# Kernel optimization log

Hardware: AMD Instinct MI355X
Metric: run time of the kernel (lower is better)

Reference implementation:

```python
import jax, jax.numpy as jnp
import numpy as np

TOP_K = 1
N_EXPERTS = 32
ALPHA = 0.001
SCALING = 1.0


def setup_inputs() -> dict:
    key = jax.random.key(0)
    k1, k2 = jax.random.split(key)
    hidden_states = jax.random.normal(k1, (16, 8192, 256), dtype=jnp.float32)
    # kaiming_uniform-ish gate weight, scale irrelevant for correctness check
    weight = jax.random.normal(k2, (32, 256), dtype=jnp.float32) * 0.06
    return {"hidden_states": hidden_states, "weight": weight}


def reference(hidden_states, weight):
    bsz, seq_len, h = hidden_states.shape
    x = hidden_states.reshape(-1, h).astype(jnp.float32)           # [N, h]
    logits = jnp.einsum('nh,eh->ne', x, weight.astype(jnp.float32))  # [N, E]
    scores = jax.nn.softmax(logits, axis=-1)
    # greedy top-k (sorted order fine; torch uses sorted=False but values identical for k=1)
    topk_weight, topk_idx = jax.lax.top_k(scores, TOP_K)            # [N, K]
    topk_weight = topk_weight * SCALING  # norm_topk_prob=False, top_k=1
    # seq_aux loss (training branch, alpha > 0)
    idx_aux = topk_idx.reshape(bsz, seq_len * TOP_K)                # [B, S*K]
    ce = jax.vmap(lambda idx: jnp.zeros((N_EXPERTS,), jnp.float32).at[idx].add(1.0))(idx_aux)
    ce = ce / (seq_len * TOP_K / N_EXPERTS)
    scores_seq = scores.reshape(bsz, seq_len, N_EXPERTS)
    aux_loss = jnp.mean(jnp.sum(ce * jnp.mean(scores_seq, axis=1), axis=1)) * ALPHA
    return topk_idx, topk_weight, aux_loss
```

## Files before the change

### kernel.cpp

```cpp
#include <hip/hip_runtime.h>
#include <math.h>

#define NTOK (16 * 8192)
#define H    256
#define E    32
#define SEQ  8192
#define BSZ  16
#define T    4

__global__ __launch_bounds__(256) void zero_ws_kernel(float* ws) {
    int i = blockIdx.x * 256 + threadIdx.x;
    if (i < BSZ * E * 2) ws[i] = 0.0f;
}

__global__ __launch_bounds__(128, 2) void gate_kernel(
    const float* __restrict__ x, const float* __restrict__ w,
    float* __restrict__ out, float* __restrict__ ws_cnt, float* __restrict__ ws_sum)
{
    __shared__ float w_lds[E * H];

    const int tid = threadIdx.x;

    {
        float4*       wl = (float4*)w_lds;
        const float4* wg = (const float4*)w;
#pragma unroll
        for (int i = 0; i < (E * H / 4) / 128; ++i)
            wl[tid + 128 * i] = wg[tid + 128 * i];
    }
    __syncthreads();

    const int lane = tid & 63;
    const int col  = lane & 31;
    const int half = lane >> 5;
    const int wavebase = blockIdx.x * 256 + (tid >> 6) * 128;
    const int tok0 = wavebase + col * T;

    const float* xbase = x + (size_t)tok0 * H + half * 128;

    float acc[E][T];
#pragma unroll
    for (int e = 0; e < E; ++e)
#pragma unroll
        for (int t = 0; t < T; ++t) acc[e][t] = 0.0f;

    float4 cur[T], nxt[T];
#pragma unroll
    for (int t = 0; t < T; ++t)
        cur[t] = *(const float4*)(xbase + t * H);

#pragma unroll 1
    for (int hc = 0; hc < 128; hc += 4) {
        const int hn = (hc + 4) & 127;
#pragma unroll
        for (int t = 0; t < T; ++t)
            nxt[t] = *(const float4*)(xbase + t * H + hn);

#pragma unroll
        for (int e = 0; e < E; ++e) {
            const float4 wv = *(const float4*)(w_lds + e * H + half * 128 + hc);
#pragma unroll
            for (int t = 0; t < T; ++t) {
                acc[e][t] += wv.x * cur[t].x + wv.y * cur[t].y
                           + wv.z * cur[t].z + wv.w * cur[t].w;
            }
        }
#pragma unroll
        for (int t = 0; t < T; ++t) cur[t] = nxt[t];
    }

#pragma unroll
    for (int e = 0; e < E; ++e)
#pragma unroll
        for (int t = 0; t < T; ++t)
            acc[e][t] += __shfl_xor(acc[e][t], 32, 64);

    float m_s[2], inv_s[2];
    int   idx_s[2];
#pragma unroll
    for (int s = 0; s < 2; ++s) {
        float m = half ? acc[0][2 + s] : acc[0][s];
        int   id = 0;
#pragma unroll
        for (int e = 1; e < E; ++e) {
            const float v = half ? acc[e][2 + s] : acc[e][s];
            if (v > m) { m = v; id = e; }
        }
        float ss = 0.0f;
#pragma unroll
        for (int e = 0; e < E; ++e) {
            const float v = half ? acc[e][2 + s] : acc[e][s];
            ss += expf(v - m);
        }
        const float inv = 1.0f / ss;
        const int token = tok0 + half * 2 + s;
        out[token]        = (float)id;
        out[NTOK + token] = inv;
        m_s[s] = m; inv_s[s] = inv; idx_s[s] = id;
    }

    const int b = wavebase >> 13;

#pragma unroll 1
    for (int e = 0; e < E; ++e) {
        const float v0 = half ? acc[e][2] : acc[e][0];
        const float v1 = half ? acc[e][3] : acc[e][1];
        float sc = expf(v0 - m_s[0]) * inv_s[0] + expf(v1 - m_s[1]) * inv_s[1];
        float cn = (float)((idx_s[0] == e) + (idx_s[1] == e));
#pragma unroll
        for (int off = 32; off > 0; off >>= 1) {
            sc += __shfl_xor(sc, off, 64);
            cn += __shfl_xor(cn, off, 64);
        }
        if (lane == 0) {
            atomicAdd(&ws_sum[b * E + e], sc);
            if (cn != 0.0f) atomicAdd(&ws_cnt[b * E + e], cn);
        }
    }
}

__global__ __launch_bounds__(256) void aux_kernel(
    const float* __restrict__ ws_cnt, const float* __restrict__ ws_sum,
    float* __restrict__ out)
{
    const int tid = threadIdx.x;
    float p = 0.0f;
    for (int i = tid; i < BSZ * E; i += 256)
        p += ws_cnt[i] * ws_sum[i];

    __shared__ float red[4];
#pragma unroll
    for (int off = 32; off > 0; off >>= 1)
        p += __shfl_xor(p, off, 64);
    if ((tid & 63) == 0) red[tid >> 6] = p;
    __syncthreads();
    if (tid == 0) {
        float t = red[0] + red[1] + red[2] + red[3];
        out[2 * NTOK] = t * (0.001f / (16.0f * 256.0f * 8192.0f));
    }
}

extern "C" void kernel_launch(void* const* d_in, const int* in_sizes, int n_in,
                              void* d_out, int out_size, void* d_ws, size_t ws_size,
                              hipStream_t stream) {
    const float* x = (const float*)d_in[0];
    const float* w = (const float*)d_in[1];
    float* out    = (float*)d_out;
    float* ws     = (float*)d_ws;
    float* ws_cnt = ws;
    float* ws_sum = ws + BSZ * E;

    zero_ws_kernel<<<4, 256, 0, stream>>>(ws);
    gate_kernel<<<NTOK / 256, 128, 0, stream>>>(x, w, out, ws_cnt, ws_sum);
    aux_kernel<<<1, 256, 0, stream>>>(ws_cnt, ws_sum, out);
}
```

Before: 271.8 us.

## Halve tokens per thread, widen blocks, deepen h-chunk, ballot-based expert counts

Each thread now handles 2 tokens instead of 4, and blocks grow to 256 threads, so each wave covers 64 tokens. The h-loop processes 8 elements per step with explicit fmaf chains, and the weight tile in LDS is reused by more waves per block. Softmax exponentials are computed once and reused for the score sums, and the per-expert counts come from a ballot plus popcount instead of a shuffle reduction. The aim is lower register pressure and higher occupancy, at the cost of less x-register reuse per weight load from LDS.

```diff
diff --git a/kernel.cpp b/kernel.cpp
--- a/kernel.cpp
+++ b/kernel.cpp
@@ -6,14 +6,14 @@
 #define E    32
 #define SEQ  8192
 #define BSZ  16
-#define T    4
+#define T    2
 
 __global__ __launch_bounds__(256) void zero_ws_kernel(float* ws) {
     int i = blockIdx.x * 256 + threadIdx.x;
     if (i < BSZ * E * 2) ws[i] = 0.0f;
 }
 
-__global__ __launch_bounds__(128, 2) void gate_kernel(
+__global__ __launch_bounds__(256, 2) void gate_kernel(
     const float* __restrict__ x, const float* __restrict__ w,
     float* __restrict__ out, float* __restrict__ ws_cnt, float* __restrict__ ws_sum)
 {
@@ -25,18 +25,19 @@
         float4*       wl = (float4*)w_lds;
         const float4* wg = (const float4*)w;
 #pragma unroll
-        for (int i = 0; i < (E * H / 4) / 128; ++i)
-            wl[tid + 128 * i] = wg[tid + 128 * i];
+        for (int i = 0; i < (E * H / 4) / 256; ++i)
+            wl[tid + 256 * i] = wg[tid + 256 * i];
     }
     __syncthreads();
 
     const int lane = tid & 63;
     const int col  = lane & 31;
     const int half = lane >> 5;
-    const int wavebase = blockIdx.x * 256 + (tid >> 6) * 128;
+    const int wavebase = blockIdx.x * 256 + (tid >> 6) * 64;
     const int tok0 = wavebase + col * T;
 
     const float* xbase = x + (size_t)tok0 * H + half * 128;
+    const float* wbase = w_lds + half * 128;
 
     float acc[E][T];
 #pragma unroll
@@ -44,29 +45,45 @@
 #pragma unroll
         for (int t = 0; t < T; ++t) acc[e][t] = 0.0f;
 
-    float4 cur[T], nxt[T];
+    float4 cur[T][2], nxt[T][2];
 #pragma unroll
     for (int t = 0; t < T; ++t)
-        cur[t] = *(const float4*)(xbase + t * H);
+#pragma unroll
+        for (int j = 0; j < 2; ++j)
+            cur[t][j] = *(const float4*)(xbase + t * H + 4 * j);
 
 #pragma unroll 1
-    for (int hc = 0; hc < 128; hc += 4) {
-        const int hn = (hc + 4) & 127;
+    for (int hc = 0; hc < 128; hc += 8) {
+        const int hn = (hc + 8) & 127;
 #pragma unroll
         for (int t = 0; t < T; ++t)
-            nxt[t] = *(const float4*)(xbase + t * H + hn);
+#pragma unroll
+            for (int j = 0; j < 2; ++j)
+                nxt[t][j] = *(const float4*)(xbase + t * H + hn + 4 * j);
 
 #pragma unroll
         for (int e = 0; e < E; ++e) {
-            const float4 wv = *(const float4*)(w_lds + e * H + half * 128 + hc);
+            const float4 w0 = *(const float4*)(wbase + e * H + hc);
+            const float4 w1 = *(const float4*)(wbase + e * H + hc + 4);
 #pragma unroll
             for (int t = 0; t < T; ++t) {
-                acc[e][t] += wv.x * cur[t].x + wv.y * cur[t].y
-                           + wv.z * cur[t].z + wv.w * cur[t].w;
+                float a = acc[e][t];
+                a = fmaf(w0.x, cur[t][0].x, a);
+                a = fmaf(w0.y, cur[t][0].y, a);
+                a = fmaf(w0.z, cur[t][0].z, a);
+                a = fmaf(w0.w, cur[t][0].w, a);
+                a = fmaf(w1.x, cur[t][1].x, a);
+                a = fmaf(w1.y, cur[t][1].y, a);
+                a = fmaf(w1.z, cur[t][1].z, a);
+                a = fmaf(w1.w, cur[t][1].w, a);
+                acc[e][t] = a;
             }
         }
 #pragma unroll
-        for (int t = 0; t < T; ++t) cur[t] = nxt[t];
+        for (int t = 0; t < T; ++t)
+#pragma unroll
+            for (int j = 0; j < 2; ++j)
+                cur[t][j] = nxt[t][j];
     }
 
 #pragma unroll
@@ -75,45 +92,40 @@
         for (int t = 0; t < T; ++t)
             acc[e][t] += __shfl_xor(acc[e][t], 32, 64);
 
-    float m_s[2], inv_s[2];
-    int   idx_s[2];
 #pragma unroll
-    for (int s = 0; s < 2; ++s) {
-        float m = half ? acc[0][2 + s] : acc[0][s];
-        int   id = 0;
+    for (int e = 0; e < E; ++e)
+        acc[e][0] = half ? acc[e][1] : acc[e][0];
+
+    float m  = acc[0][0];
+    int   id = 0;
 #pragma unroll
-        for (int e = 1; e < E; ++e) {
-            const float v = half ? acc[e][2 + s] : acc[e][s];
-            if (v > m) { m = v; id = e; }
-        }
-        float ss = 0.0f;
+    for (int e = 1; e < E; ++e) {
+        if (acc[e][0] > m) { m = acc[e][0]; id = e; }
+    }
+    float ss = 0.0f;
 #pragma unroll
-        for (int e = 0; e < E; ++e) {
-            const float v = half ? acc[e][2 + s] : acc[e][s];
-            ss += expf(v - m);
-        }
-        const float inv = 1.0f / ss;
-        const int token = tok0 + half * 2 + s;
-        out[token]        = (float)id;
-        out[NTOK + token] = inv;
-        m_s[s] = m; inv_s[s] = inv; idx_s[s] = id;
+    for (int e = 0; e < E; ++e) {
+        const float p = expf(acc[e][0] - m);
+        acc[e][0] = p;
+        ss += p;
     }
+    const float inv = 1.0f / ss;
+    const int token = tok0 + half;
+    out[token]        = (float)id;
+    out[NTOK + token] = inv;
 
     const int b = wavebase >> 13;
 
-#pragma unroll 1
+#pragma unroll
     for (int e = 0; e < E; ++e) {
-        const float v0 = half ? acc[e][2] : acc[e][0];
-        const float v1 = half ? acc[e][3] : acc[e][1];
-        float sc = expf(v0 - m_s[0]) * inv_s[0] + expf(v1 - m_s[1]) * inv_s[1];
-        float cn = (float)((idx_s[0] == e) + (idx_s[1] == e));
+        float sc = acc[e][0] * inv;
 #pragma unroll
-        for (int off = 32; off > 0; off >>= 1) {
+        for (int off = 32; off > 0; off >>= 1)
             sc += __shfl_xor(sc, off, 64);
-            cn += __shfl_xor(cn, off, 64);
-        }
+        const unsigned long long blt = __ballot(id == e);
         if (lane == 0) {
             atomicAdd(&ws_sum[b * E + e], sc);
+            const float cn = (float)__popcll(blt);
             if (cn != 0.0f) atomicAdd(&ws_cnt[b * E + e], cn);
         }
     }
@@ -151,6 +163,6 @@
     float* ws_sum = ws + BSZ * E;
 
     zero_ws_kernel<<<4, 256, 0, stream>>>(ws);
-    gate_kernel<<<NTOK / 256, 128, 0, stream>>>(x, w, out, ws_cnt, ws_sum);
+    gate_kernel<<<NTOK / 256, 256, 0, stream>>>(x, w, out, ws_cnt, ws_sum);
     aux_kernel<<<1, 256, 0, stream>>>(ws_cnt, ws_sum, out);
 }
```

Result: slower. 346.4 us (+27.4%).
